# Kernel optimization log

Measured on AMD Instinct MI355X. Metric: run time of the kernel, lower is better.

## Reference

```python
import jax, jax.numpy as jnp
import numpy as np
import math

B, T, HID = 2, 2048, 2048
NH, KVH, HD = 16, 4, 128  # num_heads, kv_heads, head_dim


def rotate_half(x):
    x1, x2 = x[..., : x.shape[-1] // 2], x[..., x.shape[-1] // 2 :]
    return jnp.concatenate([-x2, x1], axis=-1)


def setup_inputs() -> dict:
    key = jax.random.key(0)
    ks = jax.random.split(key, 6)
    hidden_states = jax.random.normal(ks[0], (B, T, HID), dtype=jnp.float32)
    # additive causal mask (0 on/below diag, -inf-ish above)
    causal = jnp.triu(jnp.full((T, T), -1e9, dtype=jnp.float32), k=1)
    attention_mask = causal[None, None, :, :]
    # real RoPE angles
    inv_freq = 1.0 / (10000.0 ** (np.arange(0, HD, 2, dtype=np.float32) / HD))
    t = np.arange(T, dtype=np.float32)
    freqs = np.einsum('t,d->td', t, inv_freq)
    emb = np.concatenate([freqs, freqs], axis=-1)  # (T, HD)
    cos = jnp.asarray(np.cos(emb))[None, None, :, :]
    sin = jnp.asarray(np.sin(emb))[None, None, :, :]
    s = 0.02
    Wq = jax.random.normal(ks[1], (HID, NH * HD), dtype=jnp.float32) * s
    Wk = jax.random.normal(ks[2], (HID, KVH * HD), dtype=jnp.float32) * s
    Wv = jax.random.normal(ks[3], (HID, KVH * HD), dtype=jnp.float32) * s
    Wo = jax.random.normal(ks[4], (HID, HID), dtype=jnp.float32) * s
    return dict(hidden_states=hidden_states, attention_mask=attention_mask,
                cos=cos, sin=sin, Wq=Wq, Wk=Wk, Wv=Wv, Wo=Wo)


def reference(hidden_states, attention_mask, cos, sin, Wq, Wk, Wv, Wo):
    b, t, _ = hidden_states.shape
    # projections; weights stored (in, out) so y = x @ W
    q = (hidden_states @ Wq).reshape(b, t, NH, HD).transpose(0, 2, 1, 3)   # (B,H,T,D)
    k = (hidden_states @ Wk).reshape(b, t, KVH, HD).transpose(0, 2, 1, 3)  # (B,Hkv,T,D)
    v = (hidden_states @ Wv).reshape(b, t, KVH, HD).transpose(0, 2, 1, 3)
    # RoPE
    c, s = cos[:, :, :t, :], sin[:, :, :t, :]
    q = q * c + rotate_half(q) * s
    k = k * c + rotate_half(k) * s
    # GQA: repeat_interleave kv heads
    rf = NH // KVH
    k = jnp.repeat(k, rf, axis=1)
    v = jnp.repeat(v, rf, axis=1)
    scores = jnp.einsum('bhtd,bhsd->bhts', q, k) / math.sqrt(HD)
    scores = scores + attention_mask
    probs = jax.nn.softmax(scores.astype(jnp.float32), axis=-1).astype(q.dtype)
    ctx = jnp.einsum('bhts,bhsd->bhtd', probs, v)
    ctx = ctx.transpose(0, 2, 1, 3).reshape(b, t, HID)
    return ctx @ Wo
```

## Files before the change

kernel.cpp:

```cpp
#include <hip/hip_runtime.h>
#include <hip/hip_bf16.h>
#include <math.h>

typedef __bf16 bf16;
typedef __bf16 bf16x4 __attribute__((ext_vector_type(4)));
typedef __bf16 bf16x8 __attribute__((ext_vector_type(8)));
typedef float f32x4 __attribute__((ext_vector_type(4)));

#define B_   2
#define T_   2048
#define HID_ 2048
#define NH_  16
#define KVH_ 4
#define HD_  128

__device__ __forceinline__ void gload_lds16(const bf16* g, bf16* l) {
    __builtin_amdgcn_global_load_lds(
        (const __attribute__((address_space(1))) unsigned int*)g,
        (__attribute__((address_space(3))) unsigned int*)l, 16, 0, 0);
}

__device__ __forceinline__ bf16x8 cat4(bf16x4 a, bf16x4 b) {
    bf16x8 r;
    #pragma unroll
    for (int i = 0; i < 4; i++) { r[i] = a[i]; r[i + 4] = b[i]; }
    return r;
}

__device__ __forceinline__ void transpose_tile(const float* __restrict__ in, bf16* __restrict__ out,
                                               int N, int rowOff, int kt, int nt) {
    __shared__ float tile[32][33];
    int k0 = kt * 32, n0 = nt * 32;
    int tx = threadIdx.x & 31, ty = threadIdx.x >> 5;
    for (int i = ty; i < 32; i += 8)
        tile[i][tx] = in[(size_t)(k0 + i) * N + n0 + tx];
    __syncthreads();
    for (int i = ty; i < 32; i += 8)
        out[(size_t)(rowOff + n0 + i) * 2048 + (k0 + tx)] = (bf16)tile[tx][i];
}

__global__ void prep(const float* __restrict__ hidden, bf16* __restrict__ hid_bf,
                     const float* __restrict__ Wq, const float* __restrict__ Wk,
                     const float* __restrict__ Wv, const float* __restrict__ Wo,
                     bf16* __restrict__ WqkvT, bf16* __restrict__ WoT) {
    int bid = blockIdx.x;
    if (bid < 8192) {
        int i = bid * 256 + threadIdx.x;
        float4 v = ((const float4*)hidden)[i];
        bf16x4 o = { (bf16)v.x, (bf16)v.y, (bf16)v.z, (bf16)v.w };
        ((bf16x4*)hid_bf)[i] = o;
    } else if (bid < 12288) {
        int t = bid - 8192;
        transpose_tile(Wq, WqkvT, 2048, 0, t & 63, t >> 6);
    } else if (bid < 13312) {
        int t = bid - 12288;
        transpose_tile(Wk, WqkvT, 512, 2048, t & 63, t >> 6);
    } else if (bid < 14336) {
        int t = bid - 13312;
        transpose_tile(Wv, WqkvT, 512, 2560, t & 63, t >> 6);
    } else {
        int t = bid - 14336;
        transpose_tile(Wo, WoT, 2048, 0, t & 63, t >> 6);
    }
}

__global__ __launch_bounds__(256, 2) void gemm_qkv_rope(
    const bf16* __restrict__ A, const bf16* __restrict__ BT,
    const float* __restrict__ cosb, const float* __restrict__ sinb,
    bf16* __restrict__ q, bf16* __restrict__ k, bf16* __restrict__ vT) {
    __shared__ __align__(16) char smem[128 * 136 * 2];
    bf16* As = (bf16*)smem;
    bf16* Bs = As + 128 * 64;
    bf16* Cs = (bf16*)smem;
    const int K = 2048;
    int bm = blockIdx.x * 128, hid = blockIdx.y, bn = hid * 128;
    int tid = threadIdx.x, lane = tid & 63, w = tid >> 6;
    int wm = (w & 1) * 64, wn = (w >> 1) * 64;
    int lm = lane & 15, quad = lane >> 4;
    int strow = tid >> 3;
    int g = (((tid & 7) ^ (strow & 7)) << 3);
    const bf16* ga = A  + (size_t)(bm + strow) * K + g;
    const bf16* gb = BT + (size_t)(bn + strow) * K + g;
    bf16* la = As + tid * 8;
    bf16* lb = Bs + tid * 8;
    f32x4 acc[4][4] = {};
    for (int k0 = 0; k0 < K; k0 += 64) {
        #pragma unroll
        for (int i = 0; i < 4; i++) {
            gload_lds16(ga + (size_t)(i * 32) * K, la + i * 2048);
            gload_lds16(gb + (size_t)(i * 32) * K, lb + i * 2048);
        }
        ga += 64; gb += 64;
        __syncthreads();
        #pragma unroll
        for (int half = 0; half < 2; half++) {
            int px = (((half * 4 + quad) ^ (lm & 7)) << 3);
            bf16x8 af[4], bfr[4];
            #pragma unroll
            for (int mt = 0; mt < 4; mt++) af[mt]  = *(const bf16x8*)&As[(wm + mt*16 + lm) * 64 + px];
            #pragma unroll
            for (int nt = 0; nt < 4; nt++) bfr[nt] = *(const bf16x8*)&Bs[(wn + nt*16 + lm) * 64 + px];
            #pragma unroll
            for (int mt = 0; mt < 4; mt++)
                #pragma unroll
                for (int nt = 0; nt < 4; nt++)
                    acc[mt][nt] = __builtin_amdgcn_mfma_f32_16x16x32_bf16(af[mt], bfr[nt], acc[mt][nt], 0, 0, 0);
        }
        __syncthreads();
    }
    #pragma unroll
    for (int mt = 0; mt < 4; mt++)
        #pragma unroll
        for (int r = 0; r < 4; r++) {
            int row = wm + mt*16 + quad*4 + r;
            #pragma unroll
            for (int nt = 0; nt < 4; nt++)
                Cs[row * 136 + wn + nt*16 + lm] = (bf16)acc[mt][nt][r];
        }
    __syncthreads();

    int b = bm >> 11, t0 = bm & 2047;
    if (hid < 20) {
        bool isq = hid < 16;
        int d = (tid & 15) * 8;
        float sgn = (d < 64) ? -1.f : 1.f;
        float scl = isq ? 0.12752965013239224f : 1.0f;
        bf16* dst = isq ? (q + ((size_t)(b * NH_ + hid) * T_) * HD_)
                        : (k + ((size_t)(b * KVH_ + (hid - 16)) * T_) * HD_);
        #pragma unroll
        for (int i = 0; i < 8; i++) {
            int row = (tid >> 4) + i * 16;
            int t = t0 + row;
            bf16x8 x  = *(const bf16x8*)&Cs[row * 136 + d];
            bf16x8 xo = *(const bf16x8*)&Cs[row * 136 + (d ^ 64)];
            bf16x8 o;
            #pragma unroll
            for (int j = 0; j < 8; j++) {
                float c = cosb[t * 128 + d + j], s = sinb[t * 128 + d + j];
                o[j] = (bf16)(((float)x[j] * c + sgn * (float)xo[j] * s) * scl);
            }
            *(bf16x8*)(dst + (size_t)t * HD_ + d) = o;
        }
    } else {
        int kvh = hid - 20;
        int t6 = (tid & 15) * 4;
        int C = 4 * (t6 >> 5) + ((t6 >> 2) & 3);
        int j0 = 4 * ((t6 >> 4) & 1);
        int pos = 8 * C + j0;
        bf16* dst = vT + (size_t)(b * KVH_ + kvh) * HD_ * T_;
        #pragma unroll
        for (int i = 0; i < 8; i++) {
            int d = (tid >> 4) + i * 16;
            #pragma unroll
            for (int half = 0; half < 2; half++) {
                int tt = half * 64 + t6;
                bf16x4 vv = { Cs[(tt+0)*136 + d], Cs[(tt+1)*136 + d],
                              Cs[(tt+2)*136 + d], Cs[(tt+3)*136 + d] };
                *(bf16x4*)(dst + (size_t)d * T_ + t0 + half * 64 + pos) = vv;
            }
        }
    }
}

__global__ __launch_bounds__(256, 2) void gemm_bf16_nt(
    const bf16* __restrict__ A, const bf16* __restrict__ BT, float* __restrict__ C,
    int M, int N, int K) {
    __shared__ __align__(16) bf16 As[128 * 64];
    __shared__ __align__(16) bf16 Bs[128 * 64];
    int bm = blockIdx.x * 128, bn = blockIdx.y * 128;
    int tid = threadIdx.x, lane = tid & 63, w = tid >> 6;
    int wm = (w & 1) * 64, wn = (w >> 1) * 64;
    int lm = lane & 15, quad = lane >> 4;
    int strow = tid >> 3;
    int g = (((tid & 7) ^ (strow & 7)) << 3);
    const bf16* ga = A  + (size_t)(bm + strow) * K + g;
    const bf16* gb = BT + (size_t)(bn + strow) * K + g;
    bf16* la = As + tid * 8;
    bf16* lb = Bs + tid * 8;
    f32x4 acc[4][4] = {};
    for (int k0 = 0; k0 < K; k0 += 64) {
        #pragma unroll
        for (int i = 0; i < 4; i++) {
            gload_lds16(ga + (size_t)(i * 32) * K, la + i * 2048);
            gload_lds16(gb + (size_t)(i * 32) * K, lb + i * 2048);
        }
        ga += 64; gb += 64;
        __syncthreads();
        #pragma unroll
        for (int half = 0; half < 2; half++) {
            int px = (((half * 4 + quad) ^ (lm & 7)) << 3);
            bf16x8 af[4], bfr[4];
            #pragma unroll
            for (int mt = 0; mt < 4; mt++) af[mt]  = *(const bf16x8*)&As[(wm + mt*16 + lm) * 64 + px];
            #pragma unroll
            for (int nt = 0; nt < 4; nt++) bfr[nt] = *(const bf16x8*)&Bs[(wn + nt*16 + lm) * 64 + px];
            #pragma unroll
            for (int mt = 0; mt < 4; mt++)
                #pragma unroll
                for (int nt = 0; nt < 4; nt++)
                    acc[mt][nt] = __builtin_amdgcn_mfma_f32_16x16x32_bf16(af[mt], bfr[nt], acc[mt][nt], 0, 0, 0);
        }
        __syncthreads();
    }
    #pragma unroll
    for (int mt = 0; mt < 4; mt++) {
        #pragma unroll
        for (int r = 0; r < 4; r++) {
            int row = bm + wm + mt*16 + quad*4 + r;
            float* cp = C + (size_t)row * N + bn + wn + lm;
            #pragma unroll
            for (int nt = 0; nt < 4; nt++)
                cp[nt*16] = acc[mt][nt][r];
        }
    }
}

__global__ __launch_bounds__(512, 2) void flash_attn(
    const bf16* __restrict__ q, const bf16* __restrict__ k, const bf16* __restrict__ vT,
    bf16* __restrict__ ctx) {
    __shared__ __align__(16) bf16 Ksb[2 * 64 * 128];
    __shared__ __align__(16) bf16 Vpb[2 * 128 * 64];
    int fid = blockIdx.x;
    int bkvh = fid & 7;
    int b = bkvh >> 2, kvh = bkvh & 3;
    int inner = fid >> 3;
    int hh = inner & 3;
    int j = inner >> 2;
    int qt = (j < 8) ? 15 - j : j - 8;
    int h = kvh * 4 + hh;
    int tid = threadIdx.x, lane = tid & 63, w = tid >> 6;
    int lm = lane & 15, quad = lane >> 4, kq = quad * 8;
    const bf16* kg = k  + (size_t)(b * KVH_ + kvh) * T_ * HD_;
    const bf16* vg = vT + (size_t)(b * KVH_ + kvh) * HD_ * T_;
    int ksl = lane >> 4;
    int vdl = lane >> 3;
    int vc  = (((lane & 7) ^ (vdl & 7)) << 3);
    int sxv1 = ((quad ^ (lm & 7)) << 3);
    int sxv2 = (((4 + quad) ^ (lm & 7)) << 3);

    int kfoB[4];
    #pragma unroll
    for (int kk = 0; kk < 4; kk++)
        kfoB[kk] = lm * 128 + (((kk * 4 + quad) ^ lm) << 3);
    int vfoB1 = lm * 64 + sxv1;
    int vfoB2 = lm * 64 + sxv2;

    auto stage = [&](int s0, int p) {
        bf16* kd = Ksb + p * (64 * 128);
        bf16* vd = Vpb + p * (128 * 64);
        #pragma unroll
        for (int i = 0; i < 2; i++) {
            int srow = w * 8 + i * 4;
            int kc = (((lane & 15) ^ ((srow & 15) + ksl)) << 3);
            gload_lds16(kg + (size_t)(s0 + srow + ksl) * HD_ + kc, kd + srow * 128);
        }
        #pragma unroll
        for (int i = 0; i < 2; i++) {
            int drow = w * 16 + i * 8;
            gload_lds16(vg + (size_t)(drow + vdl) * T_ + s0 + vc, vd + drow * 64);
        }
    };

    const bf16* qg = q + ((size_t)(b * NH_ + h) * T_ + qt*128 + w*16 + lm) * HD_;
    bf16x8 qf[4];
    #pragma unroll
    for (int kk = 0; kk < 4; kk++) qf[kk] = *(const bf16x8*)(qg + kk*32 + kq);

    f32x4 Ot[8] = {};
    float l_ = 0.f;
    int nIter = qt * 2 + 2;

    stage(0, 0);

    for (int it = 0; it < nIter; it++) {
        __syncthreads();
        if (it + 1 < nIter) stage((it + 1) * 64, (it + 1) & 1);
        int bo = (it & 1) << 13;

        f32x4 sacc[4] = {};
        __builtin_amdgcn_s_setprio(1);
        #pragma unroll
        for (int n = 0; n < 4; n++)
            #pragma unroll
            for (int kk = 0; kk < 4; kk++) {
                bf16x8 kf = *(const bf16x8*)&Ksb[bo + kfoB[kk] + n * 2048];
                sacc[n] = __builtin_amdgcn_mfma_f32_16x16x32_bf16(kf, qf[kk], sacc[n], 0, 0, 0);
            }
        __builtin_amdgcn_s_setprio(0);
        if (it >= qt * 2) {
            int sbase = (it - qt * 2) * 64;
            #pragma unroll
            for (int n = 0; n < 4; n++)
                #pragma unroll
                for (int r = 0; r < 4; r++)
                    if (sbase + n*16 + quad*4 + r > w*16 + lm) sacc[n][r] = -1e30f;
        }
        bf16x4 pt[4];
        #pragma unroll
        for (int n = 0; n < 4; n++) {
            f32x4 pe;
            #pragma unroll
            for (int r = 0; r < 4; r++) pe[r] = exp2f(sacc[n][r]);
            l_ += (pe[0] + pe[1]) + (pe[2] + pe[3]);
            #pragma unroll
            for (int r = 0; r < 4; r++) pt[n][r] = (bf16)pe[r];
        }
        bf16x8 pf01 = cat4(pt[0], pt[1]);
        bf16x8 pf23 = cat4(pt[2], pt[3]);
        __builtin_amdgcn_s_setprio(1);
        #pragma unroll
        for (int dt = 0; dt < 8; dt++) {
            bf16x8 vf01 = *(const bf16x8*)&Vpb[bo + vfoB1 + dt * 1024];
            Ot[dt] = __builtin_amdgcn_mfma_f32_16x16x32_bf16(vf01, pf01, Ot[dt], 0, 0, 0);
            bf16x8 vf23 = *(const bf16x8*)&Vpb[bo + vfoB2 + dt * 1024];
            Ot[dt] = __builtin_amdgcn_mfma_f32_16x16x32_bf16(vf23, pf23, Ot[dt], 0, 0, 0);
        }
        __builtin_amdgcn_s_setprio(0);
    }

    l_ += __shfl_xor(l_, 16);
    l_ += __shfl_xor(l_, 32);
    float linv = 1.0f / l_;
    bf16* cp = ctx + ((size_t)(b * T_) + qt*128 + w*16 + lm) * HID_ + h * HD_;
    #pragma unroll
    for (int dt = 0; dt < 8; dt++) {
        bf16x4 o4 = { (bf16)(Ot[dt][0]*linv), (bf16)(Ot[dt][1]*linv),
                      (bf16)(Ot[dt][2]*linv), (bf16)(Ot[dt][3]*linv) };
        *(bf16x4*)(cp + dt*16 + quad*4) = o4;
    }
}

extern "C" void kernel_launch(void* const* d_in, const int* in_sizes, int n_in,
                              void* d_out, int out_size, void* d_ws, size_t ws_size,
                              hipStream_t stream) {
    const float* hidden = (const float*)d_in[0];
    const float* cosb = (const float*)d_in[2];
    const float* sinb = (const float*)d_in[3];
    const float* Wq = (const float*)d_in[4];
    const float* Wk = (const float*)d_in[5];
    const float* Wv = (const float*)d_in[6];
    const float* Wo = (const float*)d_in[7];
    float* out = (float*)d_out;

    char* ws = (char*)d_ws;
    size_t off = 0;
    bf16* hid_bf = (bf16*)(ws + off); off += (size_t)4096*2048*2;
    bf16* WqkvT  = (bf16*)(ws + off); off += (size_t)3072*2048*2;
    bf16* WoT    = (bf16*)(ws + off); off += (size_t)2048*2048*2;
    bf16* qbuf   = (bf16*)(ws + off); off += (size_t)B_*NH_*T_*HD_*2;
    bf16* kbuf   = (bf16*)(ws + off); off += (size_t)B_*KVH_*T_*HD_*2;
    bf16* vtbuf  = (bf16*)(ws + off); off += (size_t)B_*KVH_*HD_*T_*2;
    bf16* ctx    = (bf16*)(ws + off); off += (size_t)4096*2048*2;

    prep<<<18432, 256, 0, stream>>>(hidden, hid_bf, Wq, Wk, Wv, Wo, WqkvT, WoT);
    gemm_qkv_rope<<<dim3(32, 24), 256, 0, stream>>>(hid_bf, WqkvT, cosb, sinb, qbuf, kbuf, vtbuf);
    flash_attn<<<512, 512, 0, stream>>>(qbuf, kbuf, vtbuf, ctx);
    gemm_bf16_nt<<<dim3(32, 16), 256, 0, stream>>>(ctx, WoT, out, 4096, 2048, 2048);
}
```

Baseline: 297.5 us.

## Software-pipeline PV matmul one iteration behind QK in flash attention

Each iteration now runs the P·V MFMAs for the previous tile while the current QK^T scores and exponentials are computed, so softmax work can overlap with matrix-core work instead of serialising. V staging goes to a triple buffer so the delayed tile stays resident while the next one loads, and a final PV step runs after the loop. This adds 16KB of LDS per block, which may reduce occupancy under the 2-blocks launch bound, and keeps probability fragments live across iterations, raising register pressure.

```diff
diff --git a/kernel.cpp b/kernel.cpp
--- a/kernel.cpp
+++ b/kernel.cpp
@@ -219,7 +219,7 @@
     const bf16* __restrict__ q, const bf16* __restrict__ k, const bf16* __restrict__ vT,
     bf16* __restrict__ ctx) {
     __shared__ __align__(16) bf16 Ksb[2 * 64 * 128];
-    __shared__ __align__(16) bf16 Vpb[2 * 128 * 64];
+    __shared__ __align__(16) bf16 Vpb[3 * 128 * 64];
     int fid = blockIdx.x;
     int bkvh = fid & 7;
     int b = bkvh >> 2, kvh = bkvh & 3;
@@ -245,9 +245,9 @@
     int vfoB1 = lm * 64 + sxv1;
     int vfoB2 = lm * 64 + sxv2;
 
-    auto stage = [&](int s0, int p) {
-        bf16* kd = Ksb + p * (64 * 128);
-        bf16* vd = Vpb + p * (128 * 64);
+    auto stage = [&](int s0, int pk, int pv) {
+        bf16* kd = Ksb + pk * 8192;
+        bf16* vd = Vpb + pv * 8192;
         #pragma unroll
         for (int i = 0; i < 2; i++) {
             int srow = w * 8 + i * 4;
@@ -270,12 +270,15 @@
     float l_ = 0.f;
     int nIter = qt * 2 + 2;
 
-    stage(0, 0);
+    bf16x8 pfA, pfB;
+    int pvbo = 0;
+
+    stage(0, 0, 0);
 
     for (int it = 0; it < nIter; it++) {
         __syncthreads();
-        if (it + 1 < nIter) stage((it + 1) * 64, (it + 1) & 1);
-        int bo = (it & 1) << 13;
+        if (it + 1 < nIter) stage((it + 1) * 64, (it + 1) & 1, (it + 1) % 3);
+        int kbo = (it & 1) << 13;
 
         f32x4 sacc[4] = {};
         __builtin_amdgcn_s_setprio(1);
@@ -283,7 +286,7 @@
         for (int n = 0; n < 4; n++)
             #pragma unroll
             for (int kk = 0; kk < 4; kk++) {
-                bf16x8 kf = *(const bf16x8*)&Ksb[bo + kfoB[kk] + n * 2048];
+                bf16x8 kf = *(const bf16x8*)&Ksb[kbo + kfoB[kk] + n * 2048];
                 sacc[n] = __builtin_amdgcn_mfma_f32_16x16x32_bf16(kf, qf[kk], sacc[n], 0, 0, 0);
             }
         __builtin_amdgcn_s_setprio(0);
@@ -305,18 +308,31 @@
             #pragma unroll
             for (int r = 0; r < 4; r++) pt[n][r] = (bf16)pe[r];
         }
-        bf16x8 pf01 = cat4(pt[0], pt[1]);
-        bf16x8 pf23 = cat4(pt[2], pt[3]);
-        __builtin_amdgcn_s_setprio(1);
-        #pragma unroll
-        for (int dt = 0; dt < 8; dt++) {
-            bf16x8 vf01 = *(const bf16x8*)&Vpb[bo + vfoB1 + dt * 1024];
-            Ot[dt] = __builtin_amdgcn_mfma_f32_16x16x32_bf16(vf01, pf01, Ot[dt], 0, 0, 0);
-            bf16x8 vf23 = *(const bf16x8*)&Vpb[bo + vfoB2 + dt * 1024];
-            Ot[dt] = __builtin_amdgcn_mfma_f32_16x16x32_bf16(vf23, pf23, Ot[dt], 0, 0, 0);
-        }
-        __builtin_amdgcn_s_setprio(0);
-    }
+        bf16x8 npfA = cat4(pt[0], pt[1]);
+        bf16x8 npfB = cat4(pt[2], pt[3]);
+        if (it > 0) {
+            __builtin_amdgcn_s_setprio(1);
+            #pragma unroll
+            for (int dt = 0; dt < 8; dt++) {
+                bf16x8 vf01 = *(const bf16x8*)&Vpb[pvbo + vfoB1 + dt * 1024];
+                Ot[dt] = __builtin_amdgcn_mfma_f32_16x16x32_bf16(vf01, pfA, Ot[dt], 0, 0, 0);
+                bf16x8 vf23 = *(const bf16x8*)&Vpb[pvbo + vfoB2 + dt * 1024];
+                Ot[dt] = __builtin_amdgcn_mfma_f32_16x16x32_bf16(vf23, pfB, Ot[dt], 0, 0, 0);
+            }
+            __builtin_amdgcn_s_setprio(0);
+        }
+        pfA = npfA; pfB = npfB;
+        pvbo = (it % 3) << 13;
+    }
+    __builtin_amdgcn_s_setprio(1);
+    #pragma unroll
+    for (int dt = 0; dt < 8; dt++) {
+        bf16x8 vf01 = *(const bf16x8*)&Vpb[pvbo + vfoB1 + dt * 1024];
+        Ot[dt] = __builtin_amdgcn_mfma_f32_16x16x32_bf16(vf01, pfA, Ot[dt], 0, 0, 0);
+        bf16x8 vf23 = *(const bf16x8*)&Vpb[pvbo + vfoB2 + dt * 1024];
+        Ot[dt] = __builtin_amdgcn_mfma_f32_16x16x32_bf16(vf23, pfB, Ot[dt], 0, 0, 0);
+    }
+    __builtin_amdgcn_s_setprio(0);
 
     l_ += __shfl_xor(l_, 16);
     l_ += __shfl_xor(l_, 32);
```

After: 290.3 us. -2.4%, faster.

## Load K fragments directly into registers and shrink attention blocks to 64 queries

Applied to the files above, without the earlier changes.

The flash attention kernel stops staging K tiles through shared memory. Each wave now loads its K MFMA fragments straight from global memory into registers, prefetching the next tile while the current one is processed, and only V stays double-buffered in LDS. Blocks shrink from 512 threads covering 128 query rows to 256 threads covering 64 rows, launched as 1024 blocks with a matching causal tile order. The aim is to cut LDS traffic and footprint and to raise occupancy and load balance. In exchange each wave issues redundant, less coalesced global K loads, and register pressure rises from the 16-fragment K buffer.

```diff
diff --git a/kernel.cpp b/kernel.cpp
--- a/kernel.cpp
+++ b/kernel.cpp
@@ -215,10 +215,9 @@
     }
 }
 
-__global__ __launch_bounds__(512, 2) void flash_attn(
+__global__ __launch_bounds__(256, 4) void flash_attn(
     const bf16* __restrict__ q, const bf16* __restrict__ k, const bf16* __restrict__ vT,
     bf16* __restrict__ ctx) {
-    __shared__ __align__(16) bf16 Ksb[2 * 64 * 128];
     __shared__ __align__(16) bf16 Vpb[2 * 128 * 64];
     int fid = blockIdx.x;
     int bkvh = fid & 7;
@@ -226,74 +225,71 @@
     int inner = fid >> 3;
     int hh = inner & 3;
     int j = inner >> 2;
-    int qt = (j < 8) ? 15 - j : j - 8;
+    int qt = (j < 16) ? 31 - j : j - 16;
     int h = kvh * 4 + hh;
     int tid = threadIdx.x, lane = tid & 63, w = tid >> 6;
     int lm = lane & 15, quad = lane >> 4, kq = quad * 8;
     const bf16* kg = k  + (size_t)(b * KVH_ + kvh) * T_ * HD_;
     const bf16* vg = vT + (size_t)(b * KVH_ + kvh) * HD_ * T_;
-    int ksl = lane >> 4;
     int vdl = lane >> 3;
     int vc  = (((lane & 7) ^ (vdl & 7)) << 3);
     int sxv1 = ((quad ^ (lm & 7)) << 3);
     int sxv2 = (((4 + quad) ^ (lm & 7)) << 3);
-
-    int kfoB[4];
-    #pragma unroll
-    for (int kk = 0; kk < 4; kk++)
-        kfoB[kk] = lm * 128 + (((kk * 4 + quad) ^ lm) << 3);
     int vfoB1 = lm * 64 + sxv1;
     int vfoB2 = lm * 64 + sxv2;
 
-    auto stage = [&](int s0, int p) {
-        bf16* kd = Ksb + p * (64 * 128);
-        bf16* vd = Vpb + p * (128 * 64);
-        #pragma unroll
-        for (int i = 0; i < 2; i++) {
-            int srow = w * 8 + i * 4;
-            int kc = (((lane & 15) ^ ((srow & 15) + ksl)) << 3);
-            gload_lds16(kg + (size_t)(s0 + srow + ksl) * HD_ + kc, kd + srow * 128);
-        }
-        #pragma unroll
-        for (int i = 0; i < 2; i++) {
-            int drow = w * 16 + i * 8;
+    const bf16* kfb = kg + lm * 128 + kq;
+
+    auto stageV = [&](int s0, int p) {
+        bf16* vd = Vpb + p * 8192;
+        #pragma unroll
+        for (int i = 0; i < 4; i++) {
+            int drow = w * 32 + i * 8;
             gload_lds16(vg + (size_t)(drow + vdl) * T_ + s0 + vc, vd + drow * 64);
         }
     };
 
-    const bf16* qg = q + ((size_t)(b * NH_ + h) * T_ + qt*128 + w*16 + lm) * HD_;
+    const bf16* qg = q + ((size_t)(b * NH_ + h) * T_ + qt*64 + w*16 + lm) * HD_;
     bf16x8 qf[4];
     #pragma unroll
     for (int kk = 0; kk < 4; kk++) qf[kk] = *(const bf16x8*)(qg + kk*32 + kq);
+
+    bf16x8 kfr[4][4];
+    auto loadK = [&](int s0) {
+        #pragma unroll
+        for (int n = 0; n < 4; n++)
+            #pragma unroll
+            for (int kk = 0; kk < 4; kk++)
+                kfr[n][kk] = *(const bf16x8*)(kfb + (size_t)(s0 + n * 16) * 128 + kk * 32);
+    };
 
     f32x4 Ot[8] = {};
     float l_ = 0.f;
-    int nIter = qt * 2 + 2;
-
-    stage(0, 0);
+    int nIter = qt + 1;
+
+    loadK(0);
+    stageV(0, 0);
 
     for (int it = 0; it < nIter; it++) {
         __syncthreads();
-        if (it + 1 < nIter) stage((it + 1) * 64, (it + 1) & 1);
-        int bo = (it & 1) << 13;
+        if (it + 1 < nIter) stageV((it + 1) * 64, (it + 1) & 1);
+        int vbo = (it & 1) << 13;
 
         f32x4 sacc[4] = {};
         __builtin_amdgcn_s_setprio(1);
         #pragma unroll
         for (int n = 0; n < 4; n++)
             #pragma unroll
-            for (int kk = 0; kk < 4; kk++) {
-                bf16x8 kf = *(const bf16x8*)&Ksb[bo + kfoB[kk] + n * 2048];
-                sacc[n] = __builtin_amdgcn_mfma_f32_16x16x32_bf16(kf, qf[kk], sacc[n], 0, 0, 0);
-            }
+            for (int kk = 0; kk < 4; kk++)
+                sacc[n] = __builtin_amdgcn_mfma_f32_16x16x32_bf16(kfr[n][kk], qf[kk], sacc[n], 0, 0, 0);
         __builtin_amdgcn_s_setprio(0);
-        if (it >= qt * 2) {
-            int sbase = (it - qt * 2) * 64;
+        if (it + 1 < nIter) loadK((it + 1) * 64);
+        if (it == qt) {
             #pragma unroll
             for (int n = 0; n < 4; n++)
                 #pragma unroll
                 for (int r = 0; r < 4; r++)
-                    if (sbase + n*16 + quad*4 + r > w*16 + lm) sacc[n][r] = -1e30f;
+                    if (n*16 + quad*4 + r > w*16 + lm) sacc[n][r] = -1e30f;
         }
         bf16x4 pt[4];
         #pragma unroll
@@ -310,9 +306,9 @@
         __builtin_amdgcn_s_setprio(1);
         #pragma unroll
         for (int dt = 0; dt < 8; dt++) {
-            bf16x8 vf01 = *(const bf16x8*)&Vpb[bo + vfoB1 + dt * 1024];
+            bf16x8 vf01 = *(const bf16x8*)&Vpb[vbo + vfoB1 + dt * 1024];
             Ot[dt] = __builtin_amdgcn_mfma_f32_16x16x32_bf16(vf01, pf01, Ot[dt], 0, 0, 0);
-            bf16x8 vf23 = *(const bf16x8*)&Vpb[bo + vfoB2 + dt * 1024];
+            bf16x8 vf23 = *(const bf16x8*)&Vpb[vbo + vfoB2 + dt * 1024];
             Ot[dt] = __builtin_amdgcn_mfma_f32_16x16x32_bf16(vf23, pf23, Ot[dt], 0, 0, 0);
         }
         __builtin_amdgcn_s_setprio(0);
@@ -321,7 +317,7 @@
     l_ += __shfl_xor(l_, 16);
     l_ += __shfl_xor(l_, 32);
     float linv = 1.0f / l_;
-    bf16* cp = ctx + ((size_t)(b * T_) + qt*128 + w*16 + lm) * HID_ + h * HD_;
+    bf16* cp = ctx + ((size_t)(b * T_) + qt*64 + w*16 + lm) * HID_ + h * HD_;
     #pragma unroll
     for (int dt = 0; dt < 8; dt++) {
         bf16x4 o4 = { (bf16)(Ot[dt][0]*linv), (bf16)(Ot[dt][1]*linv),
@@ -354,6 +350,6 @@
 
     prep<<<18432, 256, 0, stream>>>(hidden, hid_bf, Wq, Wk, Wv, Wo, WqkvT, WoT);
     gemm_qkv_rope<<<dim3(32, 24), 256, 0, stream>>>(hid_bf, WqkvT, cosb, sinb, qbuf, kbuf, vtbuf);
-    flash_attn<<<512, 512, 0, stream>>>(qbuf, kbuf, vtbuf, ctx);
+    flash_attn<<<1024, 256, 0, stream>>>(qbuf, kbuf, vtbuf, ctx);
     gemm_bf16_nt<<<dim3(32, 16), 256, 0, stream>>>(ctx, WoT, out, 4096, 2048, 2048);
 }
```

Measured after the change: 432.4 us. +45.4%, slower.

## Give each attention wave two 16-row query groups sharing K/V fragments

Applied to the files above, without the earlier changes.

Cuts the flash attention block from 8 waves to 4, with each wave now handling 32 query rows as two 16-row groups. Each K and V fragment read from LDS feeds two MFMAs instead of one, which halves LDS read traffic per FLOP. Each thread also issues twice as many staging loads. The cost is more registers for the doubled accumulators and Q fragments, and fewer waves per CU to hide latency.

```diff
diff --git a/kernel.cpp b/kernel.cpp
--- a/kernel.cpp
+++ b/kernel.cpp
@@ -215,7 +215,7 @@
     }
 }
 
-__global__ __launch_bounds__(512, 2) void flash_attn(
+__global__ __launch_bounds__(256, 2) void flash_attn(
     const bf16* __restrict__ q, const bf16* __restrict__ k, const bf16* __restrict__ vT,
     bf16* __restrict__ ctx) {
     __shared__ __align__(16) bf16 Ksb[2 * 64 * 128];
@@ -246,28 +246,31 @@
     int vfoB2 = lm * 64 + sxv2;
 
     auto stage = [&](int s0, int p) {
-        bf16* kd = Ksb + p * (64 * 128);
-        bf16* vd = Vpb + p * (128 * 64);
-        #pragma unroll
-        for (int i = 0; i < 2; i++) {
-            int srow = w * 8 + i * 4;
+        bf16* kd = Ksb + p * 8192;
+        bf16* vd = Vpb + p * 8192;
+        #pragma unroll
+        for (int i = 0; i < 4; i++) {
+            int srow = w * 16 + i * 4;
             int kc = (((lane & 15) ^ ((srow & 15) + ksl)) << 3);
             gload_lds16(kg + (size_t)(s0 + srow + ksl) * HD_ + kc, kd + srow * 128);
         }
         #pragma unroll
-        for (int i = 0; i < 2; i++) {
-            int drow = w * 16 + i * 8;
+        for (int i = 0; i < 4; i++) {
+            int drow = w * 32 + i * 8;
             gload_lds16(vg + (size_t)(drow + vdl) * T_ + s0 + vc, vd + drow * 64);
         }
     };
 
-    const bf16* qg = q + ((size_t)(b * NH_ + h) * T_ + qt*128 + w*16 + lm) * HD_;
-    bf16x8 qf[4];
-    #pragma unroll
-    for (int kk = 0; kk < 4; kk++) qf[kk] = *(const bf16x8*)(qg + kk*32 + kq);
-
-    f32x4 Ot[8] = {};
-    float l_ = 0.f;
+    bf16x8 qf[2][4];
+    #pragma unroll
+    for (int g = 0; g < 2; g++) {
+        const bf16* qg = q + ((size_t)(b * NH_ + h) * T_ + qt*128 + w*32 + g*16 + lm) * HD_;
+        #pragma unroll
+        for (int kk = 0; kk < 4; kk++) qf[g][kk] = *(const bf16x8*)(qg + kk*32 + kq);
+    }
+
+    f32x4 Ot[2][8] = {};
+    float lsum[2] = {0.f, 0.f};
     int nIter = qt * 2 + 2;
 
     stage(0, 0);
@@ -277,56 +280,69 @@
         if (it + 1 < nIter) stage((it + 1) * 64, (it + 1) & 1);
         int bo = (it & 1) << 13;
 
-        f32x4 sacc[4] = {};
+        f32x4 sacc[2][4] = {};
         __builtin_amdgcn_s_setprio(1);
         #pragma unroll
         for (int n = 0; n < 4; n++)
             #pragma unroll
             for (int kk = 0; kk < 4; kk++) {
                 bf16x8 kf = *(const bf16x8*)&Ksb[bo + kfoB[kk] + n * 2048];
-                sacc[n] = __builtin_amdgcn_mfma_f32_16x16x32_bf16(kf, qf[kk], sacc[n], 0, 0, 0);
+                sacc[0][n] = __builtin_amdgcn_mfma_f32_16x16x32_bf16(kf, qf[0][kk], sacc[0][n], 0, 0, 0);
+                sacc[1][n] = __builtin_amdgcn_mfma_f32_16x16x32_bf16(kf, qf[1][kk], sacc[1][n], 0, 0, 0);
             }
         __builtin_amdgcn_s_setprio(0);
         if (it >= qt * 2) {
             int sbase = (it - qt * 2) * 64;
             #pragma unroll
-            for (int n = 0; n < 4; n++)
-                #pragma unroll
-                for (int r = 0; r < 4; r++)
-                    if (sbase + n*16 + quad*4 + r > w*16 + lm) sacc[n][r] = -1e30f;
-        }
-        bf16x4 pt[4];
-        #pragma unroll
-        for (int n = 0; n < 4; n++) {
-            f32x4 pe;
-            #pragma unroll
-            for (int r = 0; r < 4; r++) pe[r] = exp2f(sacc[n][r]);
-            l_ += (pe[0] + pe[1]) + (pe[2] + pe[3]);
-            #pragma unroll
-            for (int r = 0; r < 4; r++) pt[n][r] = (bf16)pe[r];
-        }
-        bf16x8 pf01 = cat4(pt[0], pt[1]);
-        bf16x8 pf23 = cat4(pt[2], pt[3]);
+            for (int g = 0; g < 2; g++)
+                #pragma unroll
+                for (int n = 0; n < 4; n++)
+                    #pragma unroll
+                    for (int r = 0; r < 4; r++)
+                        if (sbase + n*16 + quad*4 + r > w*32 + g*16 + lm) sacc[g][n][r] = -1e30f;
+        }
+        bf16x8 pf01[2], pf23[2];
+        #pragma unroll
+        for (int g = 0; g < 2; g++) {
+            bf16x4 pt[4];
+            #pragma unroll
+            for (int n = 0; n < 4; n++) {
+                f32x4 pe;
+                #pragma unroll
+                for (int r = 0; r < 4; r++) pe[r] = exp2f(sacc[g][n][r]);
+                lsum[g] += (pe[0] + pe[1]) + (pe[2] + pe[3]);
+                #pragma unroll
+                for (int r = 0; r < 4; r++) pt[n][r] = (bf16)pe[r];
+            }
+            pf01[g] = cat4(pt[0], pt[1]);
+            pf23[g] = cat4(pt[2], pt[3]);
+        }
         __builtin_amdgcn_s_setprio(1);
         #pragma unroll
         for (int dt = 0; dt < 8; dt++) {
             bf16x8 vf01 = *(const bf16x8*)&Vpb[bo + vfoB1 + dt * 1024];
-            Ot[dt] = __builtin_amdgcn_mfma_f32_16x16x32_bf16(vf01, pf01, Ot[dt], 0, 0, 0);
+            Ot[0][dt] = __builtin_amdgcn_mfma_f32_16x16x32_bf16(vf01, pf01[0], Ot[0][dt], 0, 0, 0);
+            Ot[1][dt] = __builtin_amdgcn_mfma_f32_16x16x32_bf16(vf01, pf01[1], Ot[1][dt], 0, 0, 0);
             bf16x8 vf23 = *(const bf16x8*)&Vpb[bo + vfoB2 + dt * 1024];
-            Ot[dt] = __builtin_amdgcn_mfma_f32_16x16x32_bf16(vf23, pf23, Ot[dt], 0, 0, 0);
+            Ot[0][dt] = __builtin_amdgcn_mfma_f32_16x16x32_bf16(vf23, pf23[0], Ot[0][dt], 0, 0, 0);
+            Ot[1][dt] = __builtin_amdgcn_mfma_f32_16x16x32_bf16(vf23, pf23[1], Ot[1][dt], 0, 0, 0);
         }
         __builtin_amdgcn_s_setprio(0);
     }
 
-    l_ += __shfl_xor(l_, 16);
-    l_ += __shfl_xor(l_, 32);
-    float linv = 1.0f / l_;
-    bf16* cp = ctx + ((size_t)(b * T_) + qt*128 + w*16 + lm) * HID_ + h * HD_;
-    #pragma unroll
-    for (int dt = 0; dt < 8; dt++) {
-        bf16x4 o4 = { (bf16)(Ot[dt][0]*linv), (bf16)(Ot[dt][1]*linv),
-                      (bf16)(Ot[dt][2]*linv), (bf16)(Ot[dt][3]*linv) };
-        *(bf16x4*)(cp + dt*16 + quad*4) = o4;
+    #pragma unroll
+    for (int g = 0; g < 2; g++) {
+        float l_ = lsum[g];
+        l_ += __shfl_xor(l_, 16);
+        l_ += __shfl_xor(l_, 32);
+        float linv = 1.0f / l_;
+        bf16* cp = ctx + ((size_t)(b * T_) + qt*128 + w*32 + g*16 + lm) * HID_ + h * HD_;
+        #pragma unroll
+        for (int dt = 0; dt < 8; dt++) {
+            bf16x4 o4 = { (bf16)(Ot[g][dt][0]*linv), (bf16)(Ot[g][dt][1]*linv),
+                          (bf16)(Ot[g][dt][2]*linv), (bf16)(Ot[g][dt][3]*linv) };
+            *(bf16x4*)(cp + dt*16 + quad*4) = o4;
+        }
     }
 }
 
@@ -354,6 +370,6 @@
 
     prep<<<18432, 256, 0, stream>>>(hidden, hid_bf, Wq, Wk, Wv, Wo, WqkvT, WoT);
     gemm_qkv_rope<<<dim3(32, 24), 256, 0, stream>>>(hid_bf, WqkvT, cosb, sinb, qbuf, kbuf, vtbuf);
-    flash_attn<<<512, 512, 0, stream>>>(qbuf, kbuf, vtbuf, ctx);
+    flash_attn<<<512, 256, 0, stream>>>(qbuf, kbuf, vtbuf, ctx);
     gemm_bf16_nt<<<dim3(32, 16), 256, 0, stream>>>(ctx, WoT, out, 4096, 2048, 2048);
 }
```

After: 295.6 us. About the same (-0.6%).
